# Kernel optimization log

Hardware: AMD Instinct MI355X
Metric: run time of the kernel (lower is better)

## Reference

```python
import jax, jax.numpy as jnp
import numpy as np

N = 100000   # number of nodes
E = 400000   # number of edges
C = 16       # n_in_channels == n_out_channels
L = 16       # node_conv2 .. node_conv17
EPS = 1e-5   # BatchNorm eps


def _bn(h, g, b):
    # training-mode BatchNorm1d over the edge/batch axis (biased variance)
    mu = h.mean(0)
    var = h.var(0)
    return (h - mu) * jax.lax.rsqrt(var + EPS) * g + b


def setup_inputs() -> dict:
    key = jax.random.key(0)
    ks = jax.random.split(key, 6)
    return {
        "edge_features": jax.random.normal(ks[0], (E, C), jnp.float32),
        "edge_index": jax.random.randint(ks[1], (2, E), 0, N),
        "angles": jax.random.normal(ks[2], (E,), jnp.float32),
        "Wn": jax.random.normal(ks[3], (L, C, 2 * C), jnp.float32) / np.sqrt(2.0 * C),
        "bn": jnp.zeros((L, C), jnp.float32),
        "gn": jnp.ones((L, C), jnp.float32),
        "btn": jnp.zeros((L, C), jnp.float32),
        "We": jax.random.normal(ks[4], (C, 2 * C), jnp.float32) / np.sqrt(2.0 * C),
        "be": jnp.zeros((C,), jnp.float32),
        "ge": jnp.ones((C,), jnp.float32),
        "bte": jnp.zeros((C,), jnp.float32),
    }


def _forward(edge_features, edge_index, Wn, bn, gn, btn, We, be, ge, bte):
    src, dst = edge_index[0], edge_index[1]

    # EdgeConvNoNodes: init node features = mean of incident edge features (both endpoints)
    idx = jnp.concatenate([src, dst])                       # [2E]
    feats = jnp.concatenate([edge_features, edge_features], axis=0)
    deg = jax.ops.segment_sum(jnp.ones((2 * E,), edge_features.dtype), idx, N)
    x = jax.ops.segment_sum(feats, idx, N) / jnp.clip(deg, 1.0)[:, None]  # [N, C]

    # in-degree for mean aggregation of the 16 NodeConv1 layers
    deg_in = jnp.clip(jax.ops.segment_sum(jnp.ones((E,), x.dtype), dst, N), 1.0)[:, None]

    def step(x, p):
        W, b, g, bt = p
        # message: Linear(cat(x_i, x_j)) -> BN -> LeakyReLU on [E, C]
        m = jnp.concatenate([x[dst], x[src]], axis=1) @ W.T + b
        m = jax.nn.leaky_relu(_bn(m, g, bt))
        # mean aggregation at target nodes
        return jax.ops.segment_sum(m, dst, N) / deg_in, None

    x, _ = jax.lax.scan(step, x, (Wn, bn, gn, btn))

    # EdgeConv2: per-edge MLP on both edge directions, BN stats shared over [2E]
    pair = jnp.concatenate(
        [jnp.concatenate([x[src], x[dst]], axis=1),
         jnp.concatenate([x[dst], x[src]], axis=1)], axis=0)  # [2E, 2C]
    e = jax.nn.leaky_relu(_bn(pair @ We.T + be, ge, bte))      # [2E, C]
    e_fwd, e_bwd = e[:E], e[E:]
    edge_out = 0.5 * (e_fwd + e_bwd)                           # symmetric edge feature
    side_loss = jnp.mean((e_fwd - e_bwd) ** 2)                 # symmetry side loss
    return edge_out, side_loss


def reference(edge_features, edge_index, angles, Wn, bn, gn, btn, We, be, ge, bte):
    # `angles` is accepted but unused, matching the original forward
    return _forward(edge_features, edge_index, Wn, bn, gn, btn, We, be, ge, bte)
```

## Files before the change

### kernel.cpp

```cpp
#include <hip/hip_runtime.h>
#include <hip/hip_fp16.h>
#include <cstdint>
#include <cstddef>

#define NN 100000
#define EE 400000
#define CC 16
#define LL 16
#define NB 16

typedef unsigned int uint;

__device__ __forceinline__ float lrelu(float v){ return v > 0.0f ? v : 0.01f*v; }

__device__ __forceinline__ float waveSum(float v){
#pragma unroll
  for (int off = 32; off >= 1; off >>= 1) v += __shfl_xor(v, off);
  return v;
}

__device__ __forceinline__ uint pack_h2(float a, float b){
  __half2 h = __floats2half2_rn(a, b);
  return *reinterpret_cast<uint*>(&h);
}
__device__ __forceinline__ float2 unpack_h2(uint v){
  __half2 h = *reinterpret_cast<__half2*>(&v);
  return __half22float2(h);
}

__device__ __forceinline__ void unpack_row(const uint* __restrict__ xh, int n, float* f){
  const uint4* p = (const uint4*)(xh + (size_t)n*8);
  uint4 r0 = p[0], r1 = p[1];
  uint w[8] = {r0.x,r0.y,r0.z,r0.w, r1.x,r1.y,r1.z,r1.w};
#pragma unroll
  for (int q=0;q<8;q++){ float2 v = unpack_h2(w[q]); f[2*q]=v.x; f[2*q+1]=v.y; }
}

__global__ __launch_bounds__(256) void k_count(const int* __restrict__ ei,
    int* __restrict__ cdst, int* __restrict__ csrc)
{
  int t = blockIdx.x*256 + threadIdx.x;
  if (t >= EE) return;
  int s = ei[t], d = ei[EE + t];
  atomicAdd(&cdst[d], 1);
  atomicAdd(&csrc[s], 1);
}

__device__ __forceinline__ void scan_one(const int* __restrict__ cnt,
    int* __restrict__ rp, int* __restrict__ bsums, int n, int* sd)
{
  int tid = threadIdx.x;
  int base = blockIdx.x*1024 + tid*4;
  int v0=0,v1=0,v2=0,v3=0;
  if (base+0 < n) v0 = cnt[base+0];
  if (base+1 < n) v1 = cnt[base+1];
  if (base+2 < n) v2 = cnt[base+2];
  if (base+3 < n) v3 = cnt[base+3];
  int tot = v0+v1+v2+v3;
  sd[tid] = tot; __syncthreads();
  for (int off=1; off<256; off<<=1){
    int add = (tid>=off) ? sd[tid-off] : 0;
    __syncthreads();
    sd[tid] += add;
    __syncthreads();
  }
  int excl = sd[tid] - tot;
  if (base+0 < n) rp[base+0] = excl;
  if (base+1 < n) rp[base+1] = excl+v0;
  if (base+2 < n) rp[base+2] = excl+v0+v1;
  if (base+3 < n) rp[base+3] = excl+v0+v1+v2;
  if (tid==255) bsums[blockIdx.x] = sd[255];
  __syncthreads();
}

__global__ __launch_bounds__(256) void k_scan1(const int* __restrict__ ca,
    int* __restrict__ rpa, int* __restrict__ bsa,
    const int* __restrict__ cb, int* __restrict__ rpb, int* __restrict__ bsb, int n)
{
  __shared__ int sd[256];
  scan_one(ca, rpa, bsa, n, sd);
  scan_one(cb, rpb, bsb, n, sd);
}

__device__ __forceinline__ void scan2_one(const int* __restrict__ bsums,
    int* __restrict__ boff, int nseg, int* sd)
{
  int tid = threadIdx.x;
  int v = (tid < nseg) ? bsums[tid] : 0;
  sd[tid] = v; __syncthreads();
  for (int off=1; off<256; off<<=1){
    int add = (tid>=off) ? sd[tid-off] : 0;
    __syncthreads();
    sd[tid] += add;
    __syncthreads();
  }
  if (tid < nseg) boff[tid] = sd[tid] - v;
  __syncthreads();
}

__global__ __launch_bounds__(256) void k_scan2(const int* __restrict__ bsa,
    int* __restrict__ boffa, const int* __restrict__ bsb, int* __restrict__ boffb, int nseg)
{
  __shared__ int sd[256];
  scan2_one(bsa, boffa, nseg, sd);
  scan2_one(bsb, boffb, nseg, sd);
}

__global__ __launch_bounds__(256) void k_scan3(
    int* __restrict__ rpa, int* __restrict__ cura, const int* __restrict__ boffa, int totala,
    int* __restrict__ rpb, int* __restrict__ curb, const int* __restrict__ boffb, int totalb, int n)
{
  int adda = boffa[blockIdx.x];
  int addb = boffb[blockIdx.x];
  int base = blockIdx.x*1024 + threadIdx.x*4;
#pragma unroll
  for (int i=0;i<4;i++){
    if (base+i < n){
      int va = rpa[base+i] + adda; rpa[base+i] = va; cura[base+i] = va;
      int vb = rpb[base+i] + addb; rpb[base+i] = vb; curb[base+i] = vb;
    }
  }
  if (blockIdx.x==0 && threadIdx.x==0){ rpa[n] = totala; rpb[n] = totalb; }
}

__global__ __launch_bounds__(256) void k_fill(const int* __restrict__ ei,
    int* __restrict__ cur, int2* __restrict__ sdp, int* __restrict__ eidp,
    int* __restrict__ curs, int* __restrict__ lsrc)
{
  int t = blockIdx.x*256 + threadIdx.x;
  if (t >= EE) return;
  int s = ei[t], d = ei[EE + t];
  int p = atomicAdd(&cur[d], 1);
  sdp[p] = make_int2(s, d);
  eidp[p] = t;
  int ps = atomicAdd(&curs[s], 1);
  lsrc[ps] = t;
}

__global__ __launch_bounds__(256) void k_gather0(const float* __restrict__ ef,
    const int* __restrict__ eidp, const int* __restrict__ rp,
    const int* __restrict__ lsrc, const int* __restrict__ rps,
    uint* __restrict__ xh, float* __restrict__ invdeg)
{
  int t = blockIdx.x*256 + threadIdx.x;
  if (t >= NN*8) return;
  int n = t >> 3, cp = t & 7;
  int bd = rp[n], ed = rp[n+1];
  int bs = rps[n], es = rps[n+1];
  float a0 = 0.0f, a1 = 0.0f;
  for (int i=bd; i<ed; i++){
    const float2* p = (const float2*)(ef + (size_t)eidp[i]*CC + 2*cp);
    float2 v = *p;
    a0 += v.x; a1 += v.y;
  }
  for (int i=bs; i<es; i++){
    const float2* p = (const float2*)(ef + (size_t)lsrc[i]*CC + 2*cp);
    float2 v = *p;
    a0 += v.x; a1 += v.y;
  }
  float dg = fmaxf((float)((ed-bd)+(es-bs)), 1.0f);
  xh[(size_t)n*8 + cp] = pack_h2(a0/dg, a1/dg);
  if (cp == 0){
    invdeg[n] = 1.0f / fmaxf((float)(ed-bd), 1.0f);
  }
}

__global__ __launch_bounds__(128) void k_edge(const uint* __restrict__ xh,
    const int2* __restrict__ sdp,
    const float* __restrict__ W, const float* __restrict__ b,
    uint* __restrict__ mh, double* __restrict__ st)
{
  __shared__ float sW[512];
  __shared__ float sb16[16];
  __shared__ float sredS[32], sredQ[32];
  for (int i=threadIdx.x; i<512; i+=128) sW[i] = W[i];
  if (threadIdx.x < 16) sb16[threadIdx.x] = b[threadIdx.x];
  __syncthreads();

  int t = blockIdx.x*128 + threadIdx.x;
  int e0 = 2*t, e1 = 2*t+1;
  bool val = (e1 < EE);
  float acc0[16], acc1[16];
  if (val){
    int2 p0 = sdp[e0], p1 = sdp[e1];
    float xa[32], xb[32];
    unpack_row(xh, p0.y, xa);
    unpack_row(xh, p0.x, xa + 16);
    unpack_row(xh, p1.y, xb);
    unpack_row(xh, p1.x, xb + 16);
#pragma unroll
    for (int c=0;c<16;c++){
      const float* wr = sW + c*32;
      float a0 = sb16[c], a1 = sb16[c];
#pragma unroll
      for (int k=0;k<32;k++){
        float w = wr[k];
        a0 = fmaf(w, xa[k], a0);
        a1 = fmaf(w, xb[k], a1);
      }
      acc0[c]=a0; acc1[c]=a1;
    }
    uint w0[8], w1[8];
#pragma unroll
    for (int q=0;q<8;q++){
      w0[q] = pack_h2(acc0[2*q], acc0[2*q+1]);
      w1[q] = pack_h2(acc1[2*q], acc1[2*q+1]);
    }
    uint4* po0 = (uint4*)(mh + (size_t)e0*8);
    po0[0] = make_uint4(w0[0],w0[1],w0[2],w0[3]);
    po0[1] = make_uint4(w0[4],w0[5],w0[6],w0[7]);
    uint4* po1 = (uint4*)(mh + (size_t)e1*8);
    po1[0] = make_uint4(w1[0],w1[1],w1[2],w1[3]);
    po1[1] = make_uint4(w1[4],w1[5],w1[6],w1[7]);
  } else {
#pragma unroll
    for (int c=0;c<16;c++){ acc0[c]=0.0f; acc1[c]=0.0f; }
  }

  int lane = threadIdx.x & 63, w = threadIdx.x >> 6;
#pragma unroll
  for (int c=0;c<16;c++){
    float rs = acc0[c] + acc1[c];
    float rq = acc0[c]*acc0[c] + acc1[c]*acc1[c];
    rs = waveSum(rs); rq = waveSum(rq);
    if (lane == 0){ sredS[w*16+c] = rs; sredQ[w*16+c] = rq; }
  }
  __syncthreads();
  double* stb = st + (size_t)(blockIdx.x & (NB-1))*32;
  if (threadIdx.x < 16){
    int c = threadIdx.x;
    float tot = sredS[c] + sredS[16+c];
    unsafeAtomicAdd(&stb[c], (double)tot);
  } else if (threadIdx.x < 32){
    int c = threadIdx.x - 16;
    float tot = sredQ[c] + sredQ[16+c];
    unsafeAtomicAdd(&stb[16+c], (double)tot);
  }
}

template<bool LAST>
__global__ __launch_bounds__(256) void k_node(const uint* __restrict__ mh,
    const int* __restrict__ rp,
    const float* __restrict__ invdeg, const double* __restrict__ st,
    const float* __restrict__ g, const float* __restrict__ bt,
    const float* __restrict__ We, const float* __restrict__ be,
    uint* __restrict__ xhout, uint* __restrict__ uf, uint* __restrict__ vf)
{
  __shared__ float sA[16], sB[16];
  __shared__ float sW[512];
  __shared__ float sbn[16];
  __shared__ float sX[32][17];
  const int tid = threadIdx.x;
  if (LAST){
    for (int i=tid;i<512;i+=256) sW[i] = We[i];
    if (tid < 16) sbn[tid] = be[tid];
  }
  if (tid < 16){
    int c = tid;
    double S = 0.0, Q = 0.0;
#pragma unroll
    for (int k=0;k<NB;k++){ S += st[k*32 + c]; Q += st[k*32 + 16 + c]; }
    double mu  = S * (1.0/EE);
    double var = Q * (1.0/EE) - mu*mu;
    float sc = rsqrtf((float)var + 1e-5f);
    float A = sc * g[c];
    sA[c] = A; sB[c] = bt[c] - (float)mu * A;
  }
  __syncthreads();
  int t = blockIdx.x*256 + tid;
  int n = t >> 3, cp = t & 7, nl = tid >> 3;
  float A0 = sA[2*cp], B0 = sB[2*cp];
  float A1 = sA[2*cp+1], B1 = sB[2*cp+1];
  int beg = rp[n], end = rp[n+1];
  float a0 = 0.0f, a1 = 0.0f;
  for (int i=beg; i<end; i++){
    float2 v = unpack_h2(mh[(size_t)i*8 + cp]);
    a0 += lrelu(fmaf(A0, v.x, B0));
    a1 += lrelu(fmaf(A1, v.y, B1));
  }
  float iv = invdeg[n];
  float xv0 = a0*iv, xv1 = a1*iv;

  if (!LAST){
    xhout[(size_t)n*8 + cp] = pack_h2(xv0, xv1);
  } else {
    sX[nl][2*cp] = xv0; sX[nl][2*cp+1] = xv1;
    __syncthreads();
    int c0 = 2*cp, c1 = 2*cp+1;
    const float* w0 = sW + c0*32;
    const float* w1 = sW + c1*32;
    const float* xr = sX[nl];
    float u0 = sbn[c0], u1 = sbn[c1], v0 = 0.f, v1 = 0.f;
#pragma unroll
    for (int k=0;k<16;k++){
      float xv = xr[k];
      u0 = fmaf(w0[k],    xv, u0);
      v0 = fmaf(w0[16+k], xv, v0);
      u1 = fmaf(w1[k],    xv, u1);
      v1 = fmaf(w1[16+k], xv, v1);
    }
    uf[(size_t)n*8 + cp] = pack_h2(u0, u1);
    vf[(size_t)n*8 + cp] = pack_h2(v0, v1);
  }
}

__global__ __launch_bounds__(256) void k_final1(
    const uint* __restrict__ uf, const uint* __restrict__ vf,
    const int* __restrict__ ei, double* __restrict__ st)
{
  __shared__ float sredS[64], sredQ[64];
  int t = blockIdx.x*256 + threadIdx.x;
  float ls[16], lq[16];
#pragma unroll
  for (int c=0;c<16;c++){ ls[c]=0.f; lq[c]=0.f; }
  if (t < EE){
    int s = ei[t], d = ei[EE+t];
    const uint4* pus = (const uint4*)(uf + (size_t)s*8);
    const uint4* pvd = (const uint4*)(vf + (size_t)d*8);
    const uint4* pud = (const uint4*)(uf + (size_t)d*8);
    const uint4* pvs = (const uint4*)(vf + (size_t)s*8);
    uint4 us0=pus[0], us1=pus[1], vd0=pvd[0], vd1=pvd[1];
    uint4 ud0=pud[0], ud1=pud[1], vs0=pvs[0], vs1=pvs[1];
    uint usw[8]={us0.x,us0.y,us0.z,us0.w, us1.x,us1.y,us1.z,us1.w};
    uint vdw[8]={vd0.x,vd0.y,vd0.z,vd0.w, vd1.x,vd1.y,vd1.z,vd1.w};
    uint udw[8]={ud0.x,ud0.y,ud0.z,ud0.w, ud1.x,ud1.y,ud1.z,ud1.w};
    uint vsw[8]={vs0.x,vs0.y,vs0.z,vs0.w, vs1.x,vs1.y,vs1.z,vs1.w};
#pragma unroll
    for (int q=0;q<8;q++){
      float2 a = unpack_h2(usw[q]), bq = unpack_h2(vdw[q]);
      float2 cc = unpack_h2(udw[q]), dd = unpack_h2(vsw[q]);
      float f0 = a.x + bq.x, f1 = a.y + bq.y;
      float g0 = cc.x + dd.x, g1 = cc.y + dd.y;
      ls[2*q]   += f0 + g0; lq[2*q]   += f0*f0 + g0*g0;
      ls[2*q+1] += f1 + g1; lq[2*q+1] += f1*f1 + g1*g1;
    }
  }
  int lane = threadIdx.x & 63, w = threadIdx.x >> 6;
#pragma unroll
  for (int c=0;c<16;c++){
    float rs = waveSum(ls[c]);
    float rq = waveSum(lq[c]);
    if (lane == 0){ sredS[w*16+c] = rs; sredQ[w*16+c] = rq; }
  }
  __syncthreads();
  double* stb = st + (size_t)(blockIdx.x & (NB-1))*32;
  if (threadIdx.x < 16){
    int c = threadIdx.x;
    float tot = sredS[c] + sredS[16+c] + sredS[32+c] + sredS[48+c];
    unsafeAtomicAdd(&stb[c], (double)tot);
  } else if (threadIdx.x < 32){
    int c = threadIdx.x - 16;
    float tot = sredQ[c] + sredQ[16+c] + sredQ[32+c] + sredQ[48+c];
    unsafeAtomicAdd(&stb[16+c], (double)tot);
  }
}

__global__ __launch_bounds__(256) void k_final2(
    const uint* __restrict__ uf, const uint* __restrict__ vf,
    const int* __restrict__ ei, const double* __restrict__ st,
    const float* __restrict__ g, const float* __restrict__ bt,
    float* __restrict__ out, double* __restrict__ loss)
{
  __shared__ float sA[16], sB[16];
  __shared__ float sl[4];
  if (threadIdx.x < 16){
    int c = threadIdx.x;
    double S = 0.0, Q = 0.0;
#pragma unroll
    for (int k=0;k<NB;k++){ S += st[k*32 + c]; Q += st[k*32 + 16 + c]; }
    double mu  = S * (1.0/(2.0*EE));
    double var = Q * (1.0/(2.0*EE)) - mu*mu;
    float sc = rsqrtf((float)var + 1e-5f);
    float A = sc * g[c];
    sA[c] = A; sB[c] = bt[c] - (float)mu * A;
  }
  __syncthreads();

  int t = blockIdx.x*256 + threadIdx.x;
  float lsum = 0.0f;
  if (t < EE){
    int s = ei[t], d = ei[EE+t];
    const uint4* pus = (const uint4*)(uf + (size_t)s*8);
    const uint4* pvd = (const uint4*)(vf + (size_t)d*8);
    const uint4* pud = (const uint4*)(uf + (size_t)d*8);
    const uint4* pvs = (const uint4*)(vf + (size_t)s*8);
    uint4 us0=pus[0], us1=pus[1], vd0=pvd[0], vd1=pvd[1];
    uint4 ud0=pud[0], ud1=pud[1], vs0=pvs[0], vs1=pvs[1];
    uint usw[8]={us0.x,us0.y,us0.z,us0.w, us1.x,us1.y,us1.z,us1.w};
    uint vdw[8]={vd0.x,vd0.y,vd0.z,vd0.w, vd1.x,vd1.y,vd1.z,vd1.w};
    uint udw[8]={ud0.x,ud0.y,ud0.z,ud0.w, ud1.x,ud1.y,ud1.z,ud1.w};
    uint vsw[8]={vs0.x,vs0.y,vs0.z,vs0.w, vs1.x,vs1.y,vs1.z,vs1.w};
    float fo[16];
#pragma unroll
    for (int q=0;q<8;q++){
      float2 a = unpack_h2(usw[q]), bq = unpack_h2(vdw[q]);
      float2 cc = unpack_h2(udw[q]), dd = unpack_h2(vsw[q]);
      int c0 = 2*q, c1 = 2*q+1;
      float e0 = lrelu(fmaf(sA[c0], a.x + bq.x, sB[c0]));
      float b0 = lrelu(fmaf(sA[c0], cc.x + dd.x, sB[c0]));
      float e1 = lrelu(fmaf(sA[c1], a.y + bq.y, sB[c1]));
      float b1 = lrelu(fmaf(sA[c1], cc.y + dd.y, sB[c1]));
      fo[c0] = 0.5f*(e0 + b0);
      fo[c1] = 0.5f*(e1 + b1);
      float d0 = e0 - b0, d1 = e1 - b1;
      lsum = fmaf(d0, d0, lsum);
      lsum = fmaf(d1, d1, lsum);
    }
    float4* po = (float4*)(out + (size_t)t*CC);
    po[0]=make_float4(fo[0],fo[1],fo[2],fo[3]);
    po[1]=make_float4(fo[4],fo[5],fo[6],fo[7]);
    po[2]=make_float4(fo[8],fo[9],fo[10],fo[11]);
    po[3]=make_float4(fo[12],fo[13],fo[14],fo[15]);
  }
  lsum = waveSum(lsum);
  int lane = threadIdx.x & 63, w = threadIdx.x >> 6;
  if (lane == 0) sl[w] = lsum;
  __syncthreads();
  if (threadIdx.x == 0)
    unsafeAtomicAdd(&loss[blockIdx.x & (NB-1)], (double)(sl[0]+sl[1]+sl[2]+sl[3]));
}

__global__ void k_final3(float* __restrict__ out, const double* __restrict__ loss)
{
  double s = 0.0;
#pragma unroll
  for (int k=0;k<NB;k++) s += loss[k];
  out[(size_t)EE*CC] = (float)(s * (1.0/((double)EE*CC)));
}

extern "C" void kernel_launch(void* const* d_in, const int* in_sizes, int n_in,
                              void* d_out, int out_size, void* d_ws, size_t ws_size,
                              hipStream_t stream)
{
  (void)in_sizes; (void)n_in; (void)out_size; (void)ws_size;
  const float* ef  = (const float*)d_in[0];
  const int*   ei  = (const int*)d_in[1];
  const float* Wn  = (const float*)d_in[3];
  const float* bn  = (const float*)d_in[4];
  const float* gn  = (const float*)d_in[5];
  const float* btn = (const float*)d_in[6];
  const float* We  = (const float*)d_in[7];
  const float* be  = (const float*)d_in[8];
  const float* ge  = (const float*)d_in[9];
  const float* bte = (const float*)d_in[10];
  float* out = (float*)d_out;
  char* ws = (char*)d_ws;

  size_t off = 0;
  auto alloc = [&](size_t bytes)->size_t{
    size_t r = off; off = (off + bytes + 255) & ~(size_t)255; return r;
  };
  const size_t SZN = ((size_t)NN*4 + 255) & ~(size_t)255;
  size_t o_xha    = alloc((size_t)NN*8*4);
  size_t o_xhb    = alloc((size_t)NN*8*4);
  size_t o_mh     = alloc((size_t)EE*8*4);
  size_t o_uf     = alloc((size_t)NN*8*4);
  size_t o_vf     = alloc((size_t)NN*8*4);
  size_t o_cdst   = alloc((size_t)NN*4);
  size_t o_csrc   = alloc((size_t)NN*4);
  size_t o_rp     = alloc((size_t)(NN+1)*4);
  size_t o_rps    = alloc((size_t)(NN+1)*4);
  size_t o_cur    = alloc((size_t)NN*4);
  size_t o_curs   = alloc((size_t)NN*4);
  size_t o_sdp    = alloc((size_t)EE*8);
  size_t o_eidp   = alloc((size_t)EE*4);
  size_t o_lsrc   = alloc((size_t)EE*4);
  size_t o_bsum   = alloc(512);
  size_t o_bsum2  = alloc(512);
  size_t o_boff   = alloc(512);
  size_t o_boff2  = alloc(512);
  size_t o_stats  = alloc((size_t)(17*NB*32 + NB)*8);
  size_t o_invdeg = alloc((size_t)NN*4);

  uint*   xh_a    = (uint*)(ws + o_xha);
  uint*   xh_b    = (uint*)(ws + o_xhb);
  uint*   m_h     = (uint*)(ws + o_mh);
  uint*   u_f     = (uint*)(ws + o_uf);
  uint*   v_f     = (uint*)(ws + o_vf);
  int*    cdst    = (int*)(ws + o_cdst);
  int*    csrc    = (int*)(ws + o_csrc);
  int*    rp      = (int*)(ws + o_rp);
  int*    rps     = (int*)(ws + o_rps);
  int*    cur     = (int*)(ws + o_cur);
  int*    curs    = (int*)(ws + o_curs);
  int2*   sdp     = (int2*)(ws + o_sdp);
  int*    eidp    = (int*)(ws + o_eidp);
  int*    lsrc    = (int*)(ws + o_lsrc);
  int*    bsum    = (int*)(ws + o_bsum);
  int*    bsum2   = (int*)(ws + o_bsum2);
  int*    boff    = (int*)(ws + o_boff);
  int*    boff2   = (int*)(ws + o_boff2);
  double* stats   = (double*)(ws + o_stats);
  double* lossd   = stats + (size_t)17*NB*32;
  float*  invdeg  = (float*)(ws + o_invdeg);

  const int GB_E  = (EE + 255)/256;
  const int GB_E2 = (EE/2 + 127)/128;
  const int GB_N8 = (NN*8)/256;
  const int NSEG  = (NN + 1023)/1024;

  hipMemsetAsync(cdst, 0, 2*SZN, stream);
  hipMemsetAsync(stats, 0, (size_t)(17*NB*32 + NB)*8, stream);

  k_count<<<GB_E, 256, 0, stream>>>(ei, cdst, csrc);
  k_scan1<<<NSEG, 256, 0, stream>>>(cdst, rp, bsum, csrc, rps, bsum2, NN);
  k_scan2<<<1, 256, 0, stream>>>(bsum, boff, bsum2, boff2, NSEG);
  k_scan3<<<NSEG, 256, 0, stream>>>(rp, cur, boff, EE, rps, curs, boff2, EE, NN);
  k_fill<<<GB_E, 256, 0, stream>>>(ei, cur, sdp, eidp, curs, lsrc);
  k_gather0<<<GB_N8, 256, 0, stream>>>(ef, eidp, rp, lsrc, rps, xh_a, invdeg);

  uint* xc = xh_a;
  uint* xn = xh_b;
  for (int l = 0; l < LL; ++l){
    double* st = stats + (size_t)l*NB*32;
    const float* Wl = Wn + (size_t)l*CC*2*CC;
    const float* bl = bn + (size_t)l*CC;
    k_edge<<<GB_E2, 128, 0, stream>>>(xc, sdp, Wl, bl, m_h, st);
    if (l < LL-1){
      k_node<false><<<GB_N8, 256, 0, stream>>>(m_h, rp, invdeg, st,
          gn + (size_t)l*CC, btn + (size_t)l*CC, nullptr, nullptr,
          xn, nullptr, nullptr);
      uint* tmp = xc; xc = xn; xn = tmp;
    } else {
      k_node<true><<<GB_N8, 256, 0, stream>>>(m_h, rp, invdeg, st,
          gn + (size_t)l*CC, btn + (size_t)l*CC, We, be,
          nullptr, u_f, v_f);
    }
  }

  double* stF = stats + (size_t)LL*NB*32;
  k_final1<<<GB_E, 256, 0, stream>>>(u_f, v_f, ei, stF);
  k_final2<<<GB_E, 256, 0, stream>>>(u_f, v_f, ei, stF, ge, bte, out, lossd);
  k_final3<<<1, 1, 0, stream>>>(out, lossd);
}
```

Before: 764.7 us.

## Split per-edge linear into per-node U/V projections computed in node kernel

The message linear layer W·[x_dst; x_src] is decomposed into U = W_left·x + b and V = W_right·x, computed once per node (fused into the previous layer's aggregation kernel, with a standalone kernel for the first layer). The edge kernel then only gathers and adds U[dst] + V[src] and accumulates BN statistics, instead of doing a 32x16 matvec per edge. This moves the matmul from E edges to N nodes and cuts per-edge FLOPs. The cost is an extra pair of N-sized buffers written per layer, and an fp16 rounding of U and V before they are summed.

```diff
diff --git a/kernel.cpp b/kernel.cpp
--- a/kernel.cpp
+++ b/kernel.cpp
@@ -26,14 +26,6 @@
 __device__ __forceinline__ float2 unpack_h2(uint v){
   __half2 h = *reinterpret_cast<__half2*>(&v);
   return __half22float2(h);
-}
-
-__device__ __forceinline__ void unpack_row(const uint* __restrict__ xh, int n, float* f){
-  const uint4* p = (const uint4*)(xh + (size_t)n*8);
-  uint4 r0 = p[0], r1 = p[1];
-  uint w[8] = {r0.x,r0.y,r0.z,r0.w, r1.x,r1.y,r1.z,r1.w};
-#pragma unroll
-  for (int q=0;q<8;q++){ float2 v = unpack_h2(w[q]); f[2*q]=v.x; f[2*q+1]=v.y; }
 }
 
 __global__ __launch_bounds__(256) void k_count(const int* __restrict__ ei,
@@ -165,96 +157,133 @@
   }
 }
 
-__global__ __launch_bounds__(128) void k_edge(const uint* __restrict__ xh,
-    const int2* __restrict__ sdp,
+__global__ __launch_bounds__(256) void k_uv(const uint* __restrict__ xh,
     const float* __restrict__ W, const float* __restrict__ b,
-    uint* __restrict__ mh, double* __restrict__ st)
+    uint* __restrict__ u, uint* __restrict__ v)
 {
   __shared__ float sW[512];
   __shared__ float sb16[16];
-  __shared__ float sredS[32], sredQ[32];
-  for (int i=threadIdx.x; i<512; i+=128) sW[i] = W[i];
+  for (int i=threadIdx.x; i<512; i+=256) sW[i] = W[i];
   if (threadIdx.x < 16) sb16[threadIdx.x] = b[threadIdx.x];
   __syncthreads();
-
-  int t = blockIdx.x*128 + threadIdx.x;
+  int n = blockIdx.x*256 + threadIdx.x;
+  if (n >= NN) return;
+  float xr[16];
+  {
+    const uint4* p = (const uint4*)(xh + (size_t)n*8);
+    uint4 r0 = p[0], r1 = p[1];
+    uint w[8] = {r0.x,r0.y,r0.z,r0.w, r1.x,r1.y,r1.z,r1.w};
+#pragma unroll
+    for (int q=0;q<8;q++){ float2 f = unpack_h2(w[q]); xr[2*q]=f.x; xr[2*q+1]=f.y; }
+  }
+  uint up[8], vp[8];
+#pragma unroll
+  for (int q=0;q<8;q++){
+    int c0 = 2*q, c1 = 2*q+1;
+    const float* w0 = sW + c0*32;
+    const float* w1 = sW + c1*32;
+    float u0 = sb16[c0], u1 = sb16[c1], v0 = 0.f, v1 = 0.f;
+#pragma unroll
+    for (int k=0;k<16;k++){
+      float xv = xr[k];
+      u0 = fmaf(w0[k],    xv, u0);
+      v0 = fmaf(w0[16+k], xv, v0);
+      u1 = fmaf(w1[k],    xv, u1);
+      v1 = fmaf(w1[16+k], xv, v1);
+    }
+    up[q] = pack_h2(u0,u1);
+    vp[q] = pack_h2(v0,v1);
+  }
+  uint4* pu = (uint4*)(u + (size_t)n*8);
+  pu[0] = make_uint4(up[0],up[1],up[2],up[3]);
+  pu[1] = make_uint4(up[4],up[5],up[6],up[7]);
+  uint4* pv = (uint4*)(v + (size_t)n*8);
+  pv[0] = make_uint4(vp[0],vp[1],vp[2],vp[3]);
+  pv[1] = make_uint4(vp[4],vp[5],vp[6],vp[7]);
+}
+
+__global__ __launch_bounds__(256) void k_edge(
+    const uint* __restrict__ u, const uint* __restrict__ v,
+    const int2* __restrict__ sdp,
+    uint* __restrict__ mh, double* __restrict__ st)
+{
+  __shared__ float sredS[64], sredQ[64];
+  int t = blockIdx.x*256 + threadIdx.x;
   int e0 = 2*t, e1 = 2*t+1;
   bool val = (e1 < EE);
-  float acc0[16], acc1[16];
+  float ls[16], lq[16];
+#pragma unroll
+  for (int c=0;c<16;c++){ ls[c]=0.f; lq[c]=0.f; }
   if (val){
     int2 p0 = sdp[e0], p1 = sdp[e1];
-    float xa[32], xb[32];
-    unpack_row(xh, p0.y, xa);
-    unpack_row(xh, p0.x, xa + 16);
-    unpack_row(xh, p1.y, xb);
-    unpack_row(xh, p1.x, xb + 16);
-#pragma unroll
-    for (int c=0;c<16;c++){
-      const float* wr = sW + c*32;
-      float a0 = sb16[c], a1 = sb16[c];
-#pragma unroll
-      for (int k=0;k<32;k++){
-        float w = wr[k];
-        a0 = fmaf(w, xa[k], a0);
-        a1 = fmaf(w, xb[k], a1);
-      }
-      acc0[c]=a0; acc1[c]=a1;
-    }
-    uint w0[8], w1[8];
+    const uint4* pu0 = (const uint4*)(u + (size_t)p0.y*8);
+    const uint4* pv0 = (const uint4*)(v + (size_t)p0.x*8);
+    const uint4* pu1 = (const uint4*)(u + (size_t)p1.y*8);
+    const uint4* pv1 = (const uint4*)(v + (size_t)p1.x*8);
+    uint4 ua0=pu0[0], ua1=pu0[1];
+    uint4 va0=pv0[0], va1=pv0[1];
+    uint4 ub0=pu1[0], ub1=pu1[1];
+    uint4 vb0=pv1[0], vb1=pv1[1];
+    uint uw0[8]={ua0.x,ua0.y,ua0.z,ua0.w, ua1.x,ua1.y,ua1.z,ua1.w};
+    uint vw0[8]={va0.x,va0.y,va0.z,va0.w, va1.x,va1.y,va1.z,va1.w};
+    uint uw1[8]={ub0.x,ub0.y,ub0.z,ub0.w, ub1.x,ub1.y,ub1.z,ub1.w};
+    uint vw1[8]={vb0.x,vb0.y,vb0.z,vb0.w, vb1.x,vb1.y,vb1.z,vb1.w};
+    uint m0[8], m1[8];
 #pragma unroll
     for (int q=0;q<8;q++){
-      w0[q] = pack_h2(acc0[2*q], acc0[2*q+1]);
-      w1[q] = pack_h2(acc1[2*q], acc1[2*q+1]);
+      float2 fu = unpack_h2(uw0[q]);
+      float2 fv = unpack_h2(vw0[q]);
+      float x0 = fu.x + fv.x, x1 = fu.y + fv.y;
+      float2 gu = unpack_h2(uw1[q]);
+      float2 gv = unpack_h2(vw1[q]);
+      float y0 = gu.x + gv.x, y1 = gu.y + gv.y;
+      ls[2*q]   += x0 + y0; lq[2*q]   += x0*x0 + y0*y0;
+      ls[2*q+1] += x1 + y1; lq[2*q+1] += x1*x1 + y1*y1;
+      m0[q] = pack_h2(x0, x1);
+      m1[q] = pack_h2(y0, y1);
     }
     uint4* po0 = (uint4*)(mh + (size_t)e0*8);
-    po0[0] = make_uint4(w0[0],w0[1],w0[2],w0[3]);
-    po0[1] = make_uint4(w0[4],w0[5],w0[6],w0[7]);
+    po0[0] = make_uint4(m0[0],m0[1],m0[2],m0[3]);
+    po0[1] = make_uint4(m0[4],m0[5],m0[6],m0[7]);
     uint4* po1 = (uint4*)(mh + (size_t)e1*8);
-    po1[0] = make_uint4(w1[0],w1[1],w1[2],w1[3]);
-    po1[1] = make_uint4(w1[4],w1[5],w1[6],w1[7]);
-  } else {
-#pragma unroll
-    for (int c=0;c<16;c++){ acc0[c]=0.0f; acc1[c]=0.0f; }
+    po1[0] = make_uint4(m1[0],m1[1],m1[2],m1[3]);
+    po1[1] = make_uint4(m1[4],m1[5],m1[6],m1[7]);
   }
 
   int lane = threadIdx.x & 63, w = threadIdx.x >> 6;
 #pragma unroll
   for (int c=0;c<16;c++){
-    float rs = acc0[c] + acc1[c];
-    float rq = acc0[c]*acc0[c] + acc1[c]*acc1[c];
-    rs = waveSum(rs); rq = waveSum(rq);
+    float rs = waveSum(ls[c]);
+    float rq = waveSum(lq[c]);
     if (lane == 0){ sredS[w*16+c] = rs; sredQ[w*16+c] = rq; }
   }
   __syncthreads();
   double* stb = st + (size_t)(blockIdx.x & (NB-1))*32;
   if (threadIdx.x < 16){
     int c = threadIdx.x;
-    float tot = sredS[c] + sredS[16+c];
+    float tot = sredS[c] + sredS[16+c] + sredS[32+c] + sredS[48+c];
     unsafeAtomicAdd(&stb[c], (double)tot);
   } else if (threadIdx.x < 32){
     int c = threadIdx.x - 16;
-    float tot = sredQ[c] + sredQ[16+c];
+    float tot = sredQ[c] + sredQ[16+c] + sredQ[32+c] + sredQ[48+c];
     unsafeAtomicAdd(&stb[16+c], (double)tot);
   }
 }
 
-template<bool LAST>
 __global__ __launch_bounds__(256) void k_node(const uint* __restrict__ mh,
     const int* __restrict__ rp,
     const float* __restrict__ invdeg, const double* __restrict__ st,
     const float* __restrict__ g, const float* __restrict__ bt,
-    const float* __restrict__ We, const float* __restrict__ be,
-    uint* __restrict__ xhout, uint* __restrict__ uf, uint* __restrict__ vf)
+    const float* __restrict__ Wx, const float* __restrict__ bx,
+    uint* __restrict__ un, uint* __restrict__ vn)
 {
   __shared__ float sA[16], sB[16];
   __shared__ float sW[512];
   __shared__ float sbn[16];
   __shared__ float sX[32][17];
   const int tid = threadIdx.x;
-  if (LAST){
-    for (int i=tid;i<512;i+=256) sW[i] = We[i];
-    if (tid < 16) sbn[tid] = be[tid];
-  }
+  for (int i=tid;i<512;i+=256) sW[i] = Wx[i];
+  if (tid < 16) sbn[tid] = bx[tid];
   if (tid < 16){
     int c = tid;
     double S = 0.0, Q = 0.0;
@@ -279,29 +308,24 @@
     a1 += lrelu(fmaf(A1, v.y, B1));
   }
   float iv = invdeg[n];
-  float xv0 = a0*iv, xv1 = a1*iv;
-
-  if (!LAST){
-    xhout[(size_t)n*8 + cp] = pack_h2(xv0, xv1);
-  } else {
-    sX[nl][2*cp] = xv0; sX[nl][2*cp+1] = xv1;
-    __syncthreads();
-    int c0 = 2*cp, c1 = 2*cp+1;
-    const float* w0 = sW + c0*32;
-    const float* w1 = sW + c1*32;
-    const float* xr = sX[nl];
-    float u0 = sbn[c0], u1 = sbn[c1], v0 = 0.f, v1 = 0.f;
-#pragma unroll
-    for (int k=0;k<16;k++){
-      float xv = xr[k];
-      u0 = fmaf(w0[k],    xv, u0);
-      v0 = fmaf(w0[16+k], xv, v0);
-      u1 = fmaf(w1[k],    xv, u1);
-      v1 = fmaf(w1[16+k], xv, v1);
-    }
-    uf[(size_t)n*8 + cp] = pack_h2(u0, u1);
-    vf[(size_t)n*8 + cp] = pack_h2(v0, v1);
-  }
+  sX[nl][2*cp]   = a0*iv;
+  sX[nl][2*cp+1] = a1*iv;
+  __syncthreads();
+  int c0 = 2*cp, c1 = 2*cp+1;
+  const float* w0 = sW + c0*32;
+  const float* w1 = sW + c1*32;
+  const float* xr = sX[nl];
+  float u0 = sbn[c0], u1 = sbn[c1], v0 = 0.f, v1 = 0.f;
+#pragma unroll
+  for (int k=0;k<16;k++){
+    float xv = xr[k];
+    u0 = fmaf(w0[k],    xv, u0);
+    v0 = fmaf(w0[16+k], xv, v0);
+    u1 = fmaf(w1[k],    xv, u1);
+    v1 = fmaf(w1[16+k], xv, v1);
+  }
+  un[(size_t)n*8 + cp] = pack_h2(u0, u1);
+  vn[(size_t)n*8 + cp] = pack_h2(v0, v1);
 }
 
 __global__ __launch_bounds__(256) void k_final1(
@@ -451,11 +475,12 @@
     size_t r = off; off = (off + bytes + 255) & ~(size_t)255; return r;
   };
   const size_t SZN = ((size_t)NN*4 + 255) & ~(size_t)255;
-  size_t o_xha    = alloc((size_t)NN*8*4);
-  size_t o_xhb    = alloc((size_t)NN*8*4);
+  size_t o_xh     = alloc((size_t)NN*8*4);
+  size_t o_ua     = alloc((size_t)NN*8*4);
+  size_t o_va     = alloc((size_t)NN*8*4);
+  size_t o_ub     = alloc((size_t)NN*8*4);
+  size_t o_vb     = alloc((size_t)NN*8*4);
   size_t o_mh     = alloc((size_t)EE*8*4);
-  size_t o_uf     = alloc((size_t)NN*8*4);
-  size_t o_vf     = alloc((size_t)NN*8*4);
   size_t o_cdst   = alloc((size_t)NN*4);
   size_t o_csrc   = alloc((size_t)NN*4);
   size_t o_rp     = alloc((size_t)(NN+1)*4);
@@ -472,11 +497,12 @@
   size_t o_stats  = alloc((size_t)(17*NB*32 + NB)*8);
   size_t o_invdeg = alloc((size_t)NN*4);
 
-  uint*   xh_a    = (uint*)(ws + o_xha);
-  uint*   xh_b    = (uint*)(ws + o_xhb);
+  uint*   xh      = (uint*)(ws + o_xh);
+  uint*   u_a     = (uint*)(ws + o_ua);
+  uint*   v_a     = (uint*)(ws + o_va);
+  uint*   u_b     = (uint*)(ws + o_ub);
+  uint*   v_b     = (uint*)(ws + o_vb);
   uint*   m_h     = (uint*)(ws + o_mh);
-  uint*   u_f     = (uint*)(ws + o_uf);
-  uint*   v_f     = (uint*)(ws + o_vf);
   int*    cdst    = (int*)(ws + o_cdst);
   int*    csrc    = (int*)(ws + o_csrc);
   int*    rp      = (int*)(ws + o_rp);
@@ -495,8 +521,9 @@
   float*  invdeg  = (float*)(ws + o_invdeg);
 
   const int GB_E  = (EE + 255)/256;
-  const int GB_E2 = (EE/2 + 127)/128;
+  const int GB_E2 = (EE/2 + 255)/256;
   const int GB_N8 = (NN*8)/256;
+  const int GB_N  = (NN + 255)/256;
   const int NSEG  = (NN + 1023)/1024;
 
   hipMemsetAsync(cdst, 0, 2*SZN, stream);
@@ -507,29 +534,24 @@
   k_scan2<<<1, 256, 0, stream>>>(bsum, boff, bsum2, boff2, NSEG);
   k_scan3<<<NSEG, 256, 0, stream>>>(rp, cur, boff, EE, rps, curs, boff2, EE, NN);
   k_fill<<<GB_E, 256, 0, stream>>>(ei, cur, sdp, eidp, curs, lsrc);
-  k_gather0<<<GB_N8, 256, 0, stream>>>(ef, eidp, rp, lsrc, rps, xh_a, invdeg);
-
-  uint* xc = xh_a;
-  uint* xn = xh_b;
+  k_gather0<<<GB_N8, 256, 0, stream>>>(ef, eidp, rp, lsrc, rps, xh, invdeg);
+  k_uv<<<GB_N, 256, 0, stream>>>(xh, Wn, bn, u_a, v_a);
+
+  uint* uc = u_a; uint* vc = v_a;
+  uint* un = u_b; uint* vn = v_b;
   for (int l = 0; l < LL; ++l){
     double* st = stats + (size_t)l*NB*32;
-    const float* Wl = Wn + (size_t)l*CC*2*CC;
-    const float* bl = bn + (size_t)l*CC;
-    k_edge<<<GB_E2, 128, 0, stream>>>(xc, sdp, Wl, bl, m_h, st);
-    if (l < LL-1){
-      k_node<false><<<GB_N8, 256, 0, stream>>>(m_h, rp, invdeg, st,
-          gn + (size_t)l*CC, btn + (size_t)l*CC, nullptr, nullptr,
-          xn, nullptr, nullptr);
-      uint* tmp = xc; xc = xn; xn = tmp;
-    } else {
-      k_node<true><<<GB_N8, 256, 0, stream>>>(m_h, rp, invdeg, st,
-          gn + (size_t)l*CC, btn + (size_t)l*CC, We, be,
-          nullptr, u_f, v_f);
-    }
+    k_edge<<<GB_E2, 256, 0, stream>>>(uc, vc, sdp, m_h, st);
+    const float* Wx = (l < LL-1) ? (Wn + (size_t)(l+1)*CC*2*CC) : We;
+    const float* bx = (l < LL-1) ? (bn + (size_t)(l+1)*CC) : be;
+    k_node<<<GB_N8, 256, 0, stream>>>(m_h, rp, invdeg, st,
+        gn + (size_t)l*CC, btn + (size_t)l*CC, Wx, bx, un, vn);
+    uint* t1 = uc; uc = un; un = t1;
+    uint* t2 = vc; vc = vn; vn = t2;
   }
 
   double* stF = stats + (size_t)LL*NB*32;
-  k_final1<<<GB_E, 256, 0, stream>>>(u_f, v_f, ei, stF);
-  k_final2<<<GB_E, 256, 0, stream>>>(u_f, v_f, ei, stF, ge, bte, out, lossd);
+  k_final1<<<GB_E, 256, 0, stream>>>(uc, vc, ei, stF);
+  k_final2<<<GB_E, 256, 0, stream>>>(uc, vc, ei, stF, ge, bte, out, lossd);
   k_final3<<<1, 1, 0, stream>>>(out, lossd);
 }
```

Result: slower. 846.0 us (+10.6%).
